# Kernel optimization log

Measured on AMD Instinct MI355X. Metric: run time of the kernel, lower is better.

## Reference

```python
import jax, jax.numpy as jnp
import numpy as np

N_HEADS = 16
ROPE_BASE = 10000.0

def _rope_cos_sin(seq_len, head_dim):
    # freqs[t, j] = t / base**(2j/head_dim), j over head_dim//2 pairs
    inv_freq = 1.0 / (ROPE_BASE ** (jnp.arange(0, head_dim, 2, dtype=jnp.float32) / head_dim))
    t = jnp.arange(seq_len, dtype=jnp.float32)
    freqs = t[:, None] * inv_freq[None, :]          # [S, hd/2]
    return jnp.cos(freqs), jnp.sin(freqs)

def _apply_rope(x, cos, sin):
    # x: [B, S, H, hd]; pairs are interleaved (even, odd) -> complex (re, im)
    xr = x[..., 0::2]
    xi = x[..., 1::2]
    c = cos[None, :, None, :]
    s = sin[None, :, None, :]
    out_r = xr * c - xi * s
    out_i = xr * s + xi * c
    # interleave back: [..., hd/2, 2] -> [..., hd]
    return jnp.stack([out_r, out_i], axis=-1).reshape(x.shape)

def setup_inputs() -> dict:
    key = jax.random.key(0)
    ks = jax.random.split(key, 5)
    B, S, D = 2, 2048, 2048
    x = jax.random.normal(ks[0], (B, S, D), dtype=jnp.float32)
    w_scale = 0.02
    wq = jax.random.normal(ks[1], (D, D), dtype=jnp.float32) * w_scale
    wk = jax.random.normal(ks[2], (D, D), dtype=jnp.float32) * w_scale
    wv = jax.random.normal(ks[3], (D, D), dtype=jnp.float32) * w_scale
    wo = jax.random.normal(ks[4], (D, D), dtype=jnp.float32) * w_scale
    return {"x": x, "wq": wq, "wk": wk, "wv": wv, "wo": wo}

def reference(x, wq, wk, wv, wo):
    B, S, D = x.shape
    H = N_HEADS
    hd = D // H
    # QKV projections (torch Linear: y = x @ W^T)
    q = (x @ wq.T).reshape(B, S, H, hd)
    k = (x @ wk.T).reshape(B, S, H, hd)
    v = (x @ wv.T).reshape(B, S, H, hd)
    cos, sin = _rope_cos_sin(S, hd)
    q = _apply_rope(q, cos, sin)
    k = _apply_rope(k, cos, sin)
    # -> [B, H, S, hd]
    q = q.transpose(0, 2, 1, 3)
    k = k.transpose(0, 2, 1, 3)
    v = v.transpose(0, 2, 1, 3)
    scale = 1.0 / jnp.sqrt(jnp.float32(hd))
    scores = jnp.einsum('bhqd,bhkd->bhqk', q, k) * scale
    causal = jnp.tril(jnp.ones((S, S), dtype=bool))
    scores = jnp.where(causal[None, None], scores, jnp.float32(-1e30))
    probs = jax.nn.softmax(scores, axis=-1)
    attn = jnp.einsum('bhqk,bhkd->bhqd', probs, v)  # [B, H, S, hd]
    attn = attn.transpose(0, 2, 1, 3).reshape(B, S, D)
    return attn @ wo.T
```

## Files before the change

kernel.cpp:

```cpp
#include <hip/hip_runtime.h>
#include <hip/hip_bf16.h>

using bf16 = __hip_bfloat16;
typedef __attribute__((ext_vector_type(8))) short short8;
typedef __attribute__((ext_vector_type(4))) float floatx4;
typedef __attribute__((ext_vector_type(2))) float floatx2;

#define GLDS16(g, l)                                                        \
  __builtin_amdgcn_global_load_lds(                                         \
      (const __attribute__((address_space(1))) void*)(g),                   \
      (__attribute__((address_space(3))) void*)(l), 16, 0, 0)

__device__ __forceinline__ short f2b(float x) {
  union { bf16 h; short s; } u;
  u.h = __float2bfloat16(x);
  return u.s;
}
__device__ __forceinline__ void st(float* p, float v) { *p = v; }
__device__ __forceinline__ void st(bf16* p, float v) { *p = __float2bfloat16(v); }

template <int CTRL>
__device__ __forceinline__ float dpp_f(float x) {
  return __int_as_float(__builtin_amdgcn_update_dpp(
      0, __float_as_int(x), CTRL, 0xF, 0xF, true));
}
__device__ __forceinline__ float red16_max(float x) {
  x = fmaxf(x, dpp_f<0xB1>(x));
  x = fmaxf(x, dpp_f<0x4E>(x));
  x = fmaxf(x, dpp_f<0x141>(x));
  x = fmaxf(x, dpp_f<0x140>(x));
  return x;
}
__device__ __forceinline__ float red16_sum(float x) {
  x += dpp_f<0xB1>(x);
  x += dpp_f<0x4E>(x);
  x += dpp_f<0x141>(x);
  x += dpp_f<0x140>(x);
  return x;
}

__global__ void cast_kernel(const float* __restrict__ in, bf16* __restrict__ out,
                            long n) {
  long i = ((long)blockIdx.x * blockDim.x + threadIdx.x) * 8;
  if (i >= n) return;
  floatx4 a = *(const floatx4*)(in + i);
  floatx4 b = *(const floatx4*)(in + i + 4);
  short8 r;
  r[0] = f2b(a[0]); r[1] = f2b(a[1]); r[2] = f2b(a[2]); r[3] = f2b(a[3]);
  r[4] = f2b(b[0]); r[5] = f2b(b[1]); r[6] = f2b(b[2]); r[7] = f2b(b[3]);
  *(short8*)(out + i) = r;
}

__global__ void rope_tab_kernel(floatx2* __restrict__ tab) {
  const int t = blockIdx.x * blockDim.x + threadIdx.x;
  const int s = t >> 6, p = t & 63;
  const float invf = exp2f(-(float)p * (13.287712379549449f / 64.0f));
  float sn, cs;
  sincosf((float)s * invf, &sn, &cs);
  floatx2 e; e[0] = cs; e[1] = sn;
  tab[t] = e;
}

__device__ __forceinline__ void gemm_core(
    const bf16* __restrict__ A, const bf16* __restrict__ B, int K,
    long m0, long n0, bf16* As, bf16* Bs, floatx4 (&acc)[4][4])
{
  const int tid  = threadIdx.x;
  const int wave = tid >> 6;
  const int lane = tid & 63;
  const int quad = lane >> 4;
  const int l16  = lane & 15;
  const int wr = (wave >> 1) * 64;
  const int wc = (wave & 1) * 64;

  const int srow = wave * 32 + (lane >> 2);
  const int scol = (lane & 3) * 8;
  const bf16* Ag = A + (m0 + srow) * (long)K + scol;
  const bf16* Bg = B + (n0 + srow) * (long)K + scol;
  bf16* AsB = As + wave * 1024;
  bf16* BsB = Bs + wave * 1024;

#pragma unroll
  for (int mi = 0; mi < 4; mi++)
#pragma unroll
    for (int ni = 0; ni < 4; ni++) {
      floatx4 z = {0.f, 0.f, 0.f, 0.f};
      acc[mi][ni] = z;
    }

  for (int k0 = 0; k0 < K; k0 += 32) {
    GLDS16(Ag + k0,                AsB);
    GLDS16(Ag + 16 * (long)K + k0, AsB + 512);
    GLDS16(Bg + k0,                BsB);
    GLDS16(Bg + 16 * (long)K + k0, BsB + 512);
    __syncthreads();

    short8 a[4], b[4];
#pragma unroll
    for (int i = 0; i < 4; i++) {
      a[i] = *(const short8*)(As + (wr + i * 16 + l16) * 32 + quad * 8);
      b[i] = *(const short8*)(Bs + (wc + i * 16 + l16) * 32 + quad * 8);
    }
#pragma unroll
    for (int mi = 0; mi < 4; mi++)
#pragma unroll
      for (int ni = 0; ni < 4; ni++)
        acc[mi][ni] = __builtin_amdgcn_mfma_f32_16x16x32_bf16(
            a[mi], b[ni], acc[mi][ni], 0, 0, 0);
    __syncthreads();
  }
}

__global__ __launch_bounds__(256) void qkv_gemm(
    const bf16* __restrict__ A,
    const bf16* __restrict__ B0, const bf16* __restrict__ B1,
    const bf16* __restrict__ B2,
    bf16* __restrict__ C0, bf16* __restrict__ C1, bf16* __restrict__ Cvt,
    const floatx2* __restrict__ rtab,
    int M, int N, int K)
{
  __shared__ bf16 As[128 * 32];
  __shared__ bf16 Bs[128 * 32];

  const int sel = blockIdx.y >> 4;
  const long m0 = (long)blockIdx.x * 128;
  const long n0 = (long)(blockIdx.y & 15) * 128;
  const bf16* B = (sel == 0) ? B0 : ((sel == 1) ? B1 : B2);

  floatx4 acc[4][4];
  gemm_core(A, B, K, m0, n0, As, Bs, acc);

  const int tid  = threadIdx.x;
  const int wave = tid >> 6;
  const int lane = tid & 63;
  const int quad = lane >> 4;
  const int l16  = lane & 15;
  const int wr = (wave >> 1) * 64;
  const int wc = (wave & 1) * 64;

  if (sel < 2) {
    bf16* C = (sel == 0) ? C0 : C1;
    const float sgn = (l16 & 1) ? 1.0f : -1.0f;
#pragma unroll
    for (int ni = 0; ni < 4; ni++) {
      const int n = (int)n0 + wc + ni * 16 + l16;
      const int p = (n & 127) >> 1;
#pragma unroll
      for (int mi = 0; mi < 4; mi++) {
        floatx4 v = acc[mi][ni];
        const int mbase = (int)m0 + wr + mi * 16 + quad * 4;
#pragma unroll
        for (int r = 0; r < 4; r++) {
          const int spos = (mbase + r) & 2047;
          const floatx2 cssn = rtab[spos * 64 + p];
          const float pv = dpp_f<0xB1>(v[r]);
          const float outv = v[r] * cssn[0] + pv * (sgn * cssn[1]);
          st(&C[(long)(mbase + r) * N + n], outv);
        }
      }
    }
  } else {
#pragma unroll
    for (int ni = 0; ni < 4; ni++) {
      const int n = (int)n0 + wc + ni * 16 + l16;
      const int hh = n >> 7, d = n & 127;
#pragma unroll
      for (int mi = 0; mi < 4; mi++) {
        floatx4 v = acc[mi][ni];
        const int m = (int)m0 + wr + mi * 16 + quad * 4;
        const int bb = m >> 11, s = m & 2047;
        unsigned long long pk =
            (unsigned long long)(unsigned short)f2b(v[0]) |
            ((unsigned long long)(unsigned short)f2b(v[1]) << 16) |
            ((unsigned long long)(unsigned short)f2b(v[2]) << 32) |
            ((unsigned long long)(unsigned short)f2b(v[3]) << 48);
        *(unsigned long long*)(Cvt + ((long)((bb * 16 + hh) * 128 + d)) * 2048 + s) = pk;
      }
    }
  }
}

__global__ __launch_bounds__(256) void gemm_out(
    const bf16* __restrict__ A, const bf16* __restrict__ B,
    float* __restrict__ C, int M, int N, int K)
{
  __shared__ bf16 As[128 * 32];
  __shared__ bf16 Bs[128 * 32];
  const long m0 = (long)blockIdx.x * 128;
  const long n0 = (long)blockIdx.y * 128;

  floatx4 acc[4][4];
  gemm_core(A, B, K, m0, n0, As, Bs, acc);

  const int tid  = threadIdx.x;
  const int wave = tid >> 6;
  const int lane = tid & 63;
  const int quad = lane >> 4;
  const int l16  = lane & 15;
  const int wr = (wave >> 1) * 64;
  const int wc = (wave & 1) * 64;

#pragma unroll
  for (int mi = 0; mi < 4; mi++)
#pragma unroll
    for (int ni = 0; ni < 4; ni++) {
      floatx4 v = acc[mi][ni];
      const long row = m0 + wr + mi * 16 + quad * 4;
      const long col = n0 + wc + ni * 16 + l16;
#pragma unroll
      for (int r = 0; r < 4; r++)
        C[(row + r) * (long)N + col] = v[r];
    }
}

#define NEG_BIG (-30000.0f)

__global__ __launch_bounds__(256) void flash_attn(
    const bf16* __restrict__ q, const bf16* __restrict__ k,
    const bf16* __restrict__ vt, bf16* __restrict__ o, int S)
{
  __shared__ bf16 Ks[64 * 136];
  __shared__ bf16 Vt[128 * 72];
  __shared__ bf16 Ps[4][32 * 72];

  const int tid  = threadIdx.x;
  const int wave = tid >> 6;
  const int lane = tid & 63;
  const int quad = lane >> 4;
  const int l16  = lane & 15;

  const int bh = blockIdx.x;
  const int b  = bh >> 4, h = bh & 15;
  const int q0 = ((int)gridDim.y - 1 - (int)blockIdx.y) * 128;

  const bf16* Qb = q + ((long)b * S * 16 + h) * 128;
  const bf16* Kb = k + ((long)b * S * 16 + h) * 128;
  const bf16* Vg = vt + (long)bh * 128 * S;
  bf16*       Ob = o + ((long)b * S * 16 + h) * 128;

  int kr[4], kc[4], vr[4], vc[4];
#pragma unroll
  for (int it = 0; it < 4; it++) {
    const int c = tid + it * 256;
    kr[it] = c >> 4;  kc[it] = (c & 15) * 8;
    vr[it] = c >> 3;  vc[it] = (c & 7) * 8;
  }

  short8 aq[2][4];
#pragma unroll
  for (int mi = 0; mi < 2; mi++)
#pragma unroll
    for (int kt = 0; kt < 4; kt++)
      aq[mi][kt] = *(const short8*)(
          Qb + (long)(q0 + wave * 32 + mi * 16 + l16) * 2048 + kt * 32 + quad * 8);

  float m_i[2][4], l_i[2][4];
  floatx4 oacc[2][8];
  const floatx4 zero4 = {0.f, 0.f, 0.f, 0.f};
#pragma unroll
  for (int mi = 0; mi < 2; mi++) {
#pragma unroll
    for (int r = 0; r < 4; r++) { m_i[mi][r] = NEG_BIG; l_i[mi][r] = 0.f; }
#pragma unroll
    for (int dt = 0; dt < 8; dt++) oacc[mi][dt] = zero4;
  }

  const float SCL2 = 0.08838834764831845f * 1.4426950408889634f;
  const int wrow0 = q0 + wave * 32;
  const int last  = q0 + 64;

  short8 kreg[4], vreg[4];
#pragma unroll
  for (int it = 0; it < 4; it++) {
    kreg[it] = *(const short8*)(Kb + (long)kr[it] * 2048 + kc[it]);
    vreg[it] = *(const short8*)(Vg + (long)vr[it] * S + vc[it]);
  }

  for (int kt0 = 0; kt0 <= last; kt0 += 64) {
    __syncthreads();

#pragma unroll
    for (int it = 0; it < 4; it++) {
      *(short8*)(Ks + kr[it] * 136 + kc[it]) = kreg[it];
      *(short8*)(Vt + vr[it] * 72 + vc[it]) = vreg[it];
    }
    __syncthreads();

    if (kt0 < last) {
      const int n0 = kt0 + 64;
#pragma unroll
      for (int it = 0; it < 4; it++) {
        kreg[it] = *(const short8*)(Kb + (long)(n0 + kr[it]) * 2048 + kc[it]);
        vreg[it] = *(const short8*)(Vg + (long)vr[it] * S + n0 + vc[it]);
      }
    }

    if (kt0 <= wrow0 + 31) {
      floatx4 sc[2][4];
#pragma unroll
      for (int mi = 0; mi < 2; mi++)
#pragma unroll
        for (int nt = 0; nt < 4; nt++) sc[mi][nt] = zero4;
#pragma unroll
      for (int nt = 0; nt < 4; nt++)
#pragma unroll
        for (int kt = 0; kt < 4; kt++) {
          short8 bk = *(const short8*)(Ks + (nt * 16 + l16) * 136 + kt * 32 + quad * 8);
          sc[0][nt] = __builtin_amdgcn_mfma_f32_16x16x32_bf16(aq[0][kt], bk, sc[0][nt], 0, 0, 0);
          sc[1][nt] = __builtin_amdgcn_mfma_f32_16x16x32_bf16(aq[1][kt], bk, sc[1][nt], 0, 0, 0);
        }

      const bool needmask = (kt0 + 63 > wrow0);
      float alpha[2][4];
#pragma unroll
      for (int mi = 0; mi < 2; mi++) {
#pragma unroll
        for (int r = 0; r < 4; r++) {
          const int qr = wrow0 + mi * 16 + quad * 4 + r;
          float mx = NEG_BIG;
          if (needmask) {
#pragma unroll
            for (int nt = 0; nt < 4; nt++) {
              const int kc2 = kt0 + nt * 16 + l16;
              float vsc = sc[mi][nt][r] * SCL2;
              vsc = (kc2 <= qr) ? vsc : NEG_BIG;
              sc[mi][nt][r] = vsc;
              mx = fmaxf(mx, vsc);
            }
          } else {
#pragma unroll
            for (int nt = 0; nt < 4; nt++) {
              float vsc = sc[mi][nt][r] * SCL2;
              sc[mi][nt][r] = vsc;
              mx = fmaxf(mx, vsc);
            }
          }
          mx = red16_max(mx);
          const float mnew = fmaxf(m_i[mi][r], mx);

          alpha[mi][r] = exp2f(m_i[mi][r] - mnew);
          float rs = 0.f;
#pragma unroll
          for (int nt = 0; nt < 4; nt++) {
            float p = exp2f(sc[mi][nt][r] - mnew);
            sc[mi][nt][r] = p;
            rs += p;
          }
          rs = red16_sum(rs);
          l_i[mi][r] = l_i[mi][r] * alpha[mi][r] + rs;
          m_i[mi][r] = mnew;
        }
      }

#pragma unroll
      for (int mi = 0; mi < 2; mi++)
#pragma unroll
        for (int nt = 0; nt < 4; nt++)
#pragma unroll
          for (int r = 0; r < 4; r++)
            Ps[wave][(mi * 16 + quad * 4 + r) * 72 + nt * 16 + l16] =
                __float2bfloat16(sc[mi][nt][r]);

#pragma unroll
      for (int mi = 0; mi < 2; mi++)
#pragma unroll
        for (int dt = 0; dt < 8; dt++)
#pragma unroll
          for (int r = 0; r < 4; r++)
            oacc[mi][dt][r] *= alpha[mi][r];

#pragma unroll
      for (int ks = 0; ks < 2; ks++) {
        short8 ap0 = *(const short8*)(&Ps[wave][(l16) * 72 + ks * 32 + quad * 8]);
        short8 ap1 = *(const short8*)(&Ps[wave][(16 + l16) * 72 + ks * 32 + quad * 8]);
#pragma unroll
        for (int dt = 0; dt < 8; dt++) {
          short8 bv = *(const short8*)(Vt + (dt * 16 + l16) * 72 + ks * 32 + quad * 8);
          oacc[0][dt] = __builtin_amdgcn_mfma_f32_16x16x32_bf16(ap0, bv, oacc[0][dt], 0, 0, 0);
          oacc[1][dt] = __builtin_amdgcn_mfma_f32_16x16x32_bf16(ap1, bv, oacc[1][dt], 0, 0, 0);
        }
      }
    }
  }

#pragma unroll
  for (int mi = 0; mi < 2; mi++)
#pragma unroll
    for (int r = 0; r < 4; r++) {
      const float inv = 1.0f / l_i[mi][r];
      const long s = q0 + wave * 32 + mi * 16 + quad * 4 + r;
#pragma unroll
      for (int dt = 0; dt < 8; dt++)
        Ob[s * 2048 + dt * 16 + l16] = __float2bfloat16(oacc[mi][dt][r] * inv);
    }
}

extern "C" void kernel_launch(void* const* d_in, const int* in_sizes, int n_in,
                              void* d_out, int out_size, void* d_ws, size_t ws_size,
                              hipStream_t stream) {
  const float* x  = (const float*)d_in[0];
  const float* wq = (const float*)d_in[1];
  const float* wk = (const float*)d_in[2];
  const float* wv = (const float*)d_in[3];
  const float* wo = (const float*)d_in[4];
  float* out = (float*)d_out;

  const int B = 2, S = 2048, D = 2048, H = 16;
  const int M = B * S;
  const long tsz = (long)M * D;
  const long wsz = (long)D * D;

  if (ws_size < 4 * (size_t)tsz * sizeof(bf16)) return;

  bf16* qb  = (bf16*)d_ws;
  bf16* kb  = qb + tsz;
  bf16* vtb = kb + tsz;
  bf16* ab  = vtb + tsz;

  bf16* xb  = (bf16*)d_out;
  bf16* wqb = xb + tsz;
  bf16* wkb = wqb + wsz;
  bf16* wvb = ab;
  floatx2* rtab = (floatx2*)(ab + wsz);
  bf16* wob = qb;

  cast_kernel<<<(int)(tsz / 8 / 256), 256, 0, stream>>>(x,  xb,  tsz);
  cast_kernel<<<(int)(wsz / 8 / 256), 256, 0, stream>>>(wq, wqb, wsz);
  cast_kernel<<<(int)(wsz / 8 / 256), 256, 0, stream>>>(wk, wkb, wsz);
  cast_kernel<<<(int)(wsz / 8 / 256), 256, 0, stream>>>(wv, wvb, wsz);
  rope_tab_kernel<<<(S * 64) / 256, 256, 0, stream>>>(rtab);

  qkv_gemm<<<dim3(M / 128, 48), 256, 0, stream>>>(
      xb, wqb, wkb, wvb, qb, kb, vtb, rtab, M, D, D);

  flash_attn<<<dim3(B * H, S / 128), 256, 0, stream>>>(qb, kb, vtb, ab, S);

  cast_kernel<<<(int)(wsz / 8 / 256), 256, 0, stream>>>(wo, wob, wsz);
  gemm_out<<<dim3(M / 128, D / 128), 256, 0, stream>>>(ab, wob, out, M, D, D);
}
```

Measured before the change: 465.5 us.

## Rewrite projection GEMMs with 256x256 tiles, 4-stage LDS pipeline and swizzle

New measurement: 456.4 us. Within noise of the previous version (-2.0%).

```diff
diff --git a/kernel.cpp b/kernel.cpp
--- a/kernel.cpp
+++ b/kernel.cpp
@@ -10,6 +10,8 @@
   __builtin_amdgcn_global_load_lds(                                         \
       (const __attribute__((address_space(1))) void*)(g),                   \
       (__attribute__((address_space(3))) void*)(l), 16, 0, 0)
+
+#define MFMA16(a, b, c) __builtin_amdgcn_mfma_f32_16x16x32_bf16(a, b, c, 0, 0, 0)
 
 __device__ __forceinline__ short f2b(float x) {
   union { bf16 h; short s; } u;
@@ -61,57 +63,111 @@
   tab[t] = e;
 }
 
-__device__ __forceinline__ void gemm_core(
+__device__ __forceinline__ void gemm_core256(
     const bf16* __restrict__ A, const bf16* __restrict__ B, int K,
-    long m0, long n0, bf16* As, bf16* Bs, floatx4 (&acc)[4][4])
+    long m0, long n0, bf16* As, bf16* Bs, floatx4 (&acc)[8][4])
 {
   const int tid  = threadIdx.x;
   const int wave = tid >> 6;
   const int lane = tid & 63;
   const int quad = lane >> 4;
   const int l16  = lane & 15;
-  const int wr = (wave >> 1) * 64;
-  const int wc = (wave & 1) * 64;
-
-  const int srow = wave * 32 + (lane >> 2);
-  const int scol = (lane & 3) * 8;
-  const bf16* Ag = A + (m0 + srow) * (long)K + scol;
-  const bf16* Bg = B + (n0 + srow) * (long)K + scol;
-  bf16* AsB = As + wave * 1024;
-  bf16* BsB = Bs + wave * 1024;
-
-#pragma unroll
-  for (int mi = 0; mi < 4; mi++)
+  const int wr = wave >> 2;
+  const int wc = wave & 3;
+
+  long ga[2], gb[2];
+  int ldsoff[2];
+#pragma unroll
+  for (int i = 0; i < 2; i++) {
+    const int c = i * 512 + tid;
+    const int row = c >> 2;
+    const int col = (c & 3) ^ ((c >> 3) & 3);
+    ga[i] = (m0 + row) * (long)K + col * 8;
+    gb[i] = (n0 + row) * (long)K + col * 8;
+    ldsoff[i] = (i * 512 + wave * 64) * 8;
+  }
+
+  const int qs = (quad ^ ((l16 >> 1) & 3)) * 8;
+
+#pragma unroll
+  for (int mi = 0; mi < 8; mi++)
 #pragma unroll
     for (int ni = 0; ni < 4; ni++) {
       floatx4 z = {0.f, 0.f, 0.f, 0.f};
       acc[mi][ni] = z;
     }
 
-  for (int k0 = 0; k0 < K; k0 += 32) {
-    GLDS16(Ag + k0,                AsB);
-    GLDS16(Ag + 16 * (long)K + k0, AsB + 512);
-    GLDS16(Bg + k0,                BsB);
-    GLDS16(Bg + 16 * (long)K + k0, BsB + 512);
-    __syncthreads();
-
-    short8 a[4], b[4];
-#pragma unroll
-    for (int i = 0; i < 4; i++) {
-      a[i] = *(const short8*)(As + (wr + i * 16 + l16) * 32 + quad * 8);
-      b[i] = *(const short8*)(Bs + (wc + i * 16 + l16) * 32 + quad * 8);
-    }
-#pragma unroll
-    for (int mi = 0; mi < 4; mi++)
-#pragma unroll
-      for (int ni = 0; ni < 4; ni++)
-        acc[mi][ni] = __builtin_amdgcn_mfma_f32_16x16x32_bf16(
-            a[mi], b[ni], acc[mi][ni], 0, 0, 0);
-    __syncthreads();
-  }
-}
-
-__global__ __launch_bounds__(256) void qkv_gemm(
+  const int NT = K >> 5;
+
+#pragma unroll
+  for (int t = 0; t < 3; t++) {
+#pragma unroll
+    for (int i = 0; i < 2; i++) {
+      GLDS16(A + ga[i] + t * 32, As + t * 8192 + ldsoff[i]);
+      GLDS16(B + gb[i] + t * 32, Bs + t * 8192 + ldsoff[i]);
+    }
+  }
+  asm volatile("s_waitcnt vmcnt(8)" ::: "memory");
+  __builtin_amdgcn_s_barrier();
+
+  for (int t = 0; t < NT; t++) {
+    const bf16* Ab = As + (t & 3) * 8192;
+    const bf16* Bb = Bs + (t & 3) * 8192;
+    const int pf = t + 3;
+    bf16* Apf = As + (pf & 3) * 8192;
+    bf16* Bpf = Bs + (pf & 3) * 8192;
+    const long pfk = (long)pf * 32;
+    const bool do_pf = pf < NT;
+
+    short8 a[8], b0, b1;
+#pragma unroll
+    for (int mi = 0; mi < 8; mi++)
+      a[mi] = *(const short8*)(Ab + (wr * 128 + mi * 16 + l16) * 32 + qs);
+    b0 = *(const short8*)(Bb + (wc * 64 + 0 * 16 + l16) * 32 + qs);
+    b1 = *(const short8*)(Bb + (wc * 64 + 1 * 16 + l16) * 32 + qs);
+    if (do_pf) {
+      GLDS16(A + ga[0] + pfk, Apf + ldsoff[0]);
+      GLDS16(A + ga[1] + pfk, Apf + ldsoff[1]);
+    }
+    __builtin_amdgcn_s_barrier();
+    asm volatile("s_waitcnt lgkmcnt(0)" ::: "memory");
+    __builtin_amdgcn_sched_barrier(0);
+    __builtin_amdgcn_s_setprio(1);
+#pragma unroll
+    for (int mi = 0; mi < 8; mi++) {
+      acc[mi][0] = MFMA16(a[mi], b0, acc[mi][0]);
+      acc[mi][1] = MFMA16(a[mi], b1, acc[mi][1]);
+    }
+    __builtin_amdgcn_s_setprio(0);
+    __builtin_amdgcn_s_barrier();
+
+    short8 b2 = *(const short8*)(Bb + (wc * 64 + 2 * 16 + l16) * 32 + qs);
+    short8 b3 = *(const short8*)(Bb + (wc * 64 + 3 * 16 + l16) * 32 + qs);
+    if (do_pf) {
+      GLDS16(B + gb[0] + pfk, Bpf + ldsoff[0]);
+      GLDS16(B + gb[1] + pfk, Bpf + ldsoff[1]);
+    }
+    __builtin_amdgcn_s_barrier();
+    asm volatile("s_waitcnt lgkmcnt(0)" ::: "memory");
+    __builtin_amdgcn_sched_barrier(0);
+    __builtin_amdgcn_s_setprio(1);
+#pragma unroll
+    for (int mi = 0; mi < 8; mi++) {
+      acc[mi][2] = MFMA16(a[mi], b2, acc[mi][2]);
+      acc[mi][3] = MFMA16(a[mi], b3, acc[mi][3]);
+    }
+    __builtin_amdgcn_s_setprio(0);
+
+    const int staged = (pf < NT) ? pf : (NT - 1);
+    const int newer  = staged - t - 1;
+    if (newer >= 2)       asm volatile("s_waitcnt vmcnt(8)" ::: "memory");
+    else if (newer == 1)  asm volatile("s_waitcnt vmcnt(4)" ::: "memory");
+    else                  asm volatile("s_waitcnt vmcnt(0)" ::: "memory");
+    __builtin_amdgcn_s_barrier();
+  }
+}
+
+__global__ __launch_bounds__(512, 2) void qkv_gemm(
     const bf16* __restrict__ A,
     const bf16* __restrict__ B0, const bf16* __restrict__ B1,
     const bf16* __restrict__ B2,
@@ -119,36 +175,36 @@
     const floatx2* __restrict__ rtab,
     int M, int N, int K)
 {
-  __shared__ bf16 As[128 * 32];
-  __shared__ bf16 Bs[128 * 32];
-
-  const int sel = blockIdx.y >> 4;
-  const long m0 = (long)blockIdx.x * 128;
-  const long n0 = (long)(blockIdx.y & 15) * 128;
+  __shared__ __align__(16) bf16 As[4 * 8192];
+  __shared__ __align__(16) bf16 Bs[4 * 8192];
+
+  const int sel = blockIdx.y >> 3;
+  const long m0 = (long)blockIdx.x * 256;
+  const long n0 = (long)(blockIdx.y & 7) * 256;
   const bf16* B = (sel == 0) ? B0 : ((sel == 1) ? B1 : B2);
 
-  floatx4 acc[4][4];
-  gemm_core(A, B, K, m0, n0, As, Bs, acc);
+  floatx4 acc[8][4];
+  gemm_core256(A, B, K, m0, n0, As, Bs, acc);
 
   const int tid  = threadIdx.x;
   const int wave = tid >> 6;
   const int lane = tid & 63;
   const int quad = lane >> 4;
   const int l16  = lane & 15;
-  const int wr = (wave >> 1) * 64;
-  const int wc = (wave & 1) * 64;
+  const int wr = wave >> 2;
+  const int wc = wave & 3;
 
   if (sel < 2) {
     bf16* C = (sel == 0) ? C0 : C1;
     const float sgn = (l16 & 1) ? 1.0f : -1.0f;
 #pragma unroll
     for (int ni = 0; ni < 4; ni++) {
-      const int n = (int)n0 + wc + ni * 16 + l16;
+      const int n = (int)n0 + wc * 64 + ni * 16 + l16;
       const int p = (n & 127) >> 1;
 #pragma unroll
-      for (int mi = 0; mi < 4; mi++) {
+      for (int mi = 0; mi < 8; mi++) {
         floatx4 v = acc[mi][ni];
-        const int mbase = (int)m0 + wr + mi * 16 + quad * 4;
+        const int mbase = (int)m0 + wr * 128 + mi * 16 + quad * 4;
 #pragma unroll
         for (int r = 0; r < 4; r++) {
           const int spos = (mbase + r) & 2047;
@@ -162,12 +218,12 @@
   } else {
 #pragma unroll
     for (int ni = 0; ni < 4; ni++) {
-      const int n = (int)n0 + wc + ni * 16 + l16;
+      const int n = (int)n0 + wc * 64 + ni * 16 + l16;
       const int hh = n >> 7, d = n & 127;
 #pragma unroll
-      for (int mi = 0; mi < 4; mi++) {
+      for (int mi = 0; mi < 8; mi++) {
         floatx4 v = acc[mi][ni];
-        const int m = (int)m0 + wr + mi * 16 + quad * 4;
+        const int m = (int)m0 + wr * 128 + mi * 16 + quad * 4;
         const int bb = m >> 11, s = m & 2047;
         unsigned long long pk =
             (unsigned long long)(unsigned short)f2b(v[0]) |
@@ -180,33 +236,33 @@
   }
 }
 
-__global__ __launch_bounds__(256) void gemm_out(
+__global__ __launch_bounds__(512, 2) void gemm_out(
     const bf16* __restrict__ A, const bf16* __restrict__ B,
     float* __restrict__ C, int M, int N, int K)
 {
-  __shared__ bf16 As[128 * 32];
-  __shared__ bf16 Bs[128 * 32];
-  const long m0 = (long)blockIdx.x * 128;
-  const long n0 = (long)blockIdx.y * 128;
-
-  floatx4 acc[4][4];
-  gemm_core(A, B, K, m0, n0, As, Bs, acc);
+  __shared__ __align__(16) bf16 As[4 * 8192];
+  __shared__ __align__(16) bf16 Bs[4 * 8192];
+  const long m0 = (long)blockIdx.x * 256;
+  const long n0 = (long)blockIdx.y * 256;
+
+  floatx4 acc[8][4];
+  gemm_core256(A, B, K, m0, n0, As, Bs, acc);
 
   const int tid  = threadIdx.x;
   const int wave = tid >> 6;
   const int lane = tid & 63;
   const int quad = lane >> 4;
   const int l16  = lane & 15;
-  const int wr = (wave >> 1) * 64;
-  const int wc = (wave & 1) * 64;
-
-#pragma unroll
-  for (int mi = 0; mi < 4; mi++)
+  const int wr = wave >> 2;
+  const int wc = wave & 3;
+
+#pragma unroll
+  for (int mi = 0; mi < 8; mi++)
 #pragma unroll
     for (int ni = 0; ni < 4; ni++) {
       floatx4 v = acc[mi][ni];
-      const long row = m0 + wr + mi * 16 + quad * 4;
-      const long col = n0 + wc + ni * 16 + l16;
+      const long row = m0 + wr * 128 + mi * 16 + quad * 4;
+      const long col = n0 + wc * 64 + ni * 16 + l16;
 #pragma unroll
       for (int r = 0; r < 4; r++)
         C[(row + r) * (long)N + col] = v[r];
@@ -430,11 +486,11 @@
   cast_kernel<<<(int)(wsz / 8 / 256), 256, 0, stream>>>(wv, wvb, wsz);
   rope_tab_kernel<<<(S * 64) / 256, 256, 0, stream>>>(rtab);
 
-  qkv_gemm<<<dim3(M / 128, 48), 256, 0, stream>>>(
+  qkv_gemm<<<dim3(M / 256, 24), 512, 0, stream>>>(
       xb, wqb, wkb, wvb, qb, kb, vtb, rtab, M, D, D);
 
   flash_attn<<<dim3(B * H, S / 128), 256, 0, stream>>>(qb, kb, vtb, ab, S);
 
   cast_kernel<<<(int)(wsz / 8 / 256), 256, 0, stream>>>(wo, wob, wsz);
-  gemm_out<<<dim3(M / 128, D / 128), 256, 0, stream>>>(ab, wob, out, M, D, D);
-}
+  gemm_out<<<dim3(M / 256, D / 256), 512, 0, stream>>>(ab, wob, out, M, D, D);
+}
```
